# Optimization experiments

Measured on AMD Instinct MI355X. Metric: run time of the kernel, lower is better.

Reference implementation:

```python
import jax, jax.numpy as jnp
import numpy as np

B, S, D, F, E, K = 2, 2048, 1024, 4096, 8, 2

def setup_inputs() -> dict:
    key = jax.random.key(0)
    ks = jax.random.split(key, 5)
    x = jax.random.normal(ks[0], (B, S, D), dtype=jnp.float32)
    Wg = jax.random.normal(ks[1], (D, E), dtype=jnp.float32) * 0.02   # gate (fp32)
    W1 = jax.random.normal(ks[2], (E, D, F), dtype=jnp.float32) * 0.02  # expert fc1
    b1 = jnp.zeros((E, F), dtype=jnp.float32)
    W2 = jax.random.normal(ks[3], (E, F, D), dtype=jnp.float32) * 0.02  # expert fc2
    b2 = jnp.zeros((E, D), dtype=jnp.float32)
    return {"x": x, "Wg": Wg, "W1": W1, "b1": b1, "W2": W2, "b2": b2}

def reference(x, Wg, W1, b1, W2, b2):
    b, s, d = x.shape
    e = Wg.shape[1]
    T = b * s
    C = (2 * K * T) // e  # generous capacity -> effectively no token drops
    xt = x.reshape(T, d)

    # --- top-2 gating (fp32) ---
    logits = xt.astype(jnp.float32) @ Wg.astype(jnp.float32)  # [T,E]
    gates = jax.nn.softmax(logits, axis=-1)
    idx1 = jnp.argmax(gates, axis=-1)                      # [T]
    mask1 = jax.nn.one_hot(idx1, e, dtype=gates.dtype)     # [T,E]
    gate1 = jnp.sum(gates * mask1, axis=-1)                # [T]
    logits2 = jnp.where(mask1 > 0, -jnp.inf, logits)
    idx2 = jnp.argmax(logits2, axis=-1)
    mask2 = jax.nn.one_hot(idx2, e, dtype=gates.dtype)
    gate2 = jnp.sum(gates * mask2, axis=-1)
    denom = gate1 + gate2 + 1e-9
    w1 = gate1 / denom
    w2 = gate2 / denom

    # --- capacity-based slot assignment (GShard-style) ---
    p1 = jnp.cumsum(mask1, axis=0) - mask1                 # earlier same-expert tokens
    pos1 = jnp.sum(p1 * mask1, axis=-1).astype(jnp.int32)  # [T]
    off = jnp.sum(mask1, axis=0)                           # [E] 1st-choice counts
    p2 = jnp.cumsum(mask2, axis=0) - mask2 + off[None, :]
    pos2 = jnp.sum(p2 * mask2, axis=-1).astype(jnp.int32)
    keep1 = (pos1 < C).astype(xt.dtype)
    keep2 = (pos2 < C).astype(xt.dtype)
    pos1 = jnp.clip(pos1, 0, C - 1)
    pos2 = jnp.clip(pos2, 0, C - 1)

    # --- dispatch (scatter tokens to expert slots) ---
    xe = jnp.zeros((e, C, d), dtype=xt.dtype)
    xe = xe.at[idx1, pos1].add(xt * keep1[:, None])
    xe = xe.at[idx2, pos2].add(xt * keep2[:, None])

    # --- grouped expert FFN: gelu(x W1 + b1) W2 + b2 ---
    h = jax.nn.gelu(jnp.einsum('ecd,edf->ecf', xe, W1) + b1[:, None, :], approximate=False)
    ye = jnp.einsum('ecf,efd->ecd', h, W2) + b2[:, None, :]  # [E,C,D]

    # --- combine (gather + weighted sum) ---
    out = ye[idx1, pos1] * (w1 * keep1)[:, None] + ye[idx2, pos2] * (w2 * keep2)[:, None]
    return out.reshape(b, s, d)
```

## Files before the change

kernel.cpp:

```cpp
#include <hip/hip_runtime.h>
#include <hip/hip_bf16.h>
#include <math.h>

#define Dv 1024
#define Fv 4096
#define Ev 8
#define Tt 4096
#define CAP 2048

typedef unsigned int u32;
typedef __bf16 bf16x8 __attribute__((ext_vector_type(8)));
typedef float f32x4 __attribute__((ext_vector_type(4)));

__device__ __forceinline__ unsigned short f2bf(float f) {
  u32 u = __float_as_uint(f);
  u32 r = (u + 0x7fffu + ((u >> 16) & 1u)) >> 16;
  return (unsigned short)r;
}

__device__ __forceinline__ void gload_lds16(const void* g, void* l) {
  __builtin_amdgcn_global_load_lds(
      (const __attribute__((address_space(1))) u32*)g,
      (__attribute__((address_space(3))) u32*)l, 16, 0, 0);
}

__global__ void __launch_bounds__(256)
transpose_bf16_kernel(const float* __restrict__ src, unsigned short* __restrict__ dst,
                      int R, int Cc) {
  __shared__ float tile[64][65];
  int e = blockIdx.z;
  src += (size_t)e * R * Cc;
  dst += (size_t)e * R * Cc;
  int c0 = blockIdx.x * 64, r0 = blockIdx.y * 64;
  int tc = threadIdx.x & 63, tr = threadIdx.x >> 6;
#pragma unroll
  for (int i = tr; i < 64; i += 4)
    tile[i][tc] = src[(size_t)(r0 + i) * Cc + (c0 + tc)];
  __syncthreads();
  int rp = (threadIdx.x & 31) * 2, co = threadIdx.x >> 5;
#pragma unroll
  for (int k = 0; k < 8; ++k) {
    int c = co + 8 * k;
    ushort2 v;
    v.x = f2bf(tile[rp][c]);
    v.y = f2bf(tile[rp + 1][c]);
    *(ushort2*)&dst[(size_t)(c0 + c) * R + (r0 + rp)] = v;
  }
}

__global__ void __launch_bounds__(256)
gating_kernel(const float* __restrict__ x, const float* __restrict__ Wg,
              int* __restrict__ idx1, int* __restrict__ idx2,
              float* __restrict__ w1, float* __restrict__ w2) {
  int t = blockIdx.x * 4 + (threadIdx.x >> 6);
  int lane = threadIdx.x & 63;
  const float* xr = x + (size_t)t * Dv;
  float acc[Ev];
#pragma unroll
  for (int e = 0; e < Ev; ++e) acc[e] = 0.f;
#pragma unroll
  for (int j = 0; j < 4; ++j) {
    int dbase = (lane + 64 * j) * 4;
    float4 xv = *(const float4*)(xr + dbase);
    const float* wr = Wg + (size_t)dbase * Ev;
#pragma unroll
    for (int u = 0; u < 4; ++u) {
      float xd = (&xv.x)[u];
#pragma unroll
      for (int e = 0; e < Ev; ++e) acc[e] += xd * wr[u * Ev + e];
    }
  }
#pragma unroll
  for (int off = 32; off > 0; off >>= 1) {
#pragma unroll
    for (int e = 0; e < Ev; ++e) acc[e] += __shfl_xor(acc[e], off, 64);
  }
  if (lane == 0) {
    float mx = acc[0]; int i1 = 0;
#pragma unroll
    for (int e = 1; e < Ev; ++e) { if (acc[e] > mx) { mx = acc[e]; i1 = e; } }
    float ge[Ev]; float se = 0.f;
#pragma unroll
    for (int e = 0; e < Ev; ++e) { ge[e] = expf(acc[e] - mx); se += ge[e]; }
    float mx2 = -INFINITY; int i2 = 0; bool have = false;
#pragma unroll
    for (int e = 0; e < Ev; ++e) {
      if (e == i1) continue;
      if (!have || acc[e] > mx2) { mx2 = acc[e]; i2 = e; have = true; }
    }
    float g1 = 0.f, g2 = 0.f;
#pragma unroll
    for (int e = 0; e < Ev; ++e) { if (e == i1) g1 = ge[e]; if (e == i2) g2 = ge[e]; }
    g1 /= se; g2 /= se;
    float denom = g1 + g2 + 1e-9f;
    idx1[t] = i1; idx2[t] = i2;
    w1[t] = g1 / denom; w2[t] = g2 / denom;
  }
}

__global__ void __launch_bounds__(256)
scan_kernel(const int* __restrict__ gidx1, const int* __restrict__ gidx2,
            const float* __restrict__ gw1, const float* __restrict__ gw2,
            int* __restrict__ pos1, int* __restrict__ pos2,
            float* __restrict__ w1k, float* __restrict__ w2k,
            int* __restrict__ n_e) {
  __shared__ short s1[Tt], s2[Tt];
  __shared__ int c1[256][Ev], c2[256][Ev];
  __shared__ int tot1[Ev], tot2[Ev];
  int tid = threadIdx.x;
  for (int i = tid; i < Tt; i += 256) { s1[i] = (short)gidx1[i]; s2[i] = (short)gidx2[i]; }
  __syncthreads();
  int base = tid * 16;
  {
    int l1[Ev], l2[Ev];
#pragma unroll
    for (int e = 0; e < Ev; ++e) { l1[e] = 0; l2[e] = 0; }
    for (int j = 0; j < 16; ++j) {
      int a = s1[base + j], b = s2[base + j];
#pragma unroll
      for (int e = 0; e < Ev; ++e) { l1[e] += (a == e); l2[e] += (b == e); }
    }
#pragma unroll
    for (int e = 0; e < Ev; ++e) { c1[tid][e] = l1[e]; c2[tid][e] = l2[e]; }
  }
  __syncthreads();
  if (tid < Ev) {
    int run = 0;
    for (int c = 0; c < 256; ++c) { int v = c1[c][tid]; c1[c][tid] = run; run += v; }
    tot1[tid] = run;
  } else if (tid < 2 * Ev) {
    int e = tid - Ev; int run = 0;
    for (int c = 0; c < 256; ++c) { int v = c2[c][e]; c2[c][e] = run; run += v; }
    tot2[e] = run;
  }
  __syncthreads();
  if (tid < Ev) {
    int ne = tot1[tid] + tot2[tid];
    n_e[tid] = ne < CAP ? ne : CAP;
  }
  int r1[Ev], r2[Ev];
#pragma unroll
  for (int e = 0; e < Ev; ++e) { r1[e] = c1[tid][e]; r2[e] = c2[tid][e] + tot1[e]; }
  for (int j = 0; j < 16; ++j) {
    int tk = base + j;
    int e1 = s1[tk], e2 = s2[tk];
    int p1 = 0, p2 = 0;
#pragma unroll
    for (int e = 0; e < Ev; ++e) {
      if (e == e1) { p1 = r1[e]; r1[e]++; }
      if (e == e2) { p2 = r2[e]; r2[e]++; }
    }
    bool k1 = p1 < CAP, k2 = p2 < CAP;
    pos1[tk] = k1 ? p1 : -1;
    pos2[tk] = k2 ? p2 : -1;
    w1k[tk] = k1 ? gw1[tk] : 0.f;
    w2k[tk] = k2 ? gw2[tk] : 0.f;
  }
}

__global__ void __launch_bounds__(256)
dispatch_kernel(const float* __restrict__ x,
                const int* __restrict__ idx1, const int* __restrict__ idx2,
                const int* __restrict__ pos1, const int* __restrict__ pos2,
                unsigned short* __restrict__ Xe) {
  int t = blockIdx.x, tid = threadIdx.x;
  float4 xv = *(const float4*)(x + (size_t)t * Dv + tid * 4);
  ushort4 bv;
  bv.x = f2bf(xv.x); bv.y = f2bf(xv.y); bv.z = f2bf(xv.z); bv.w = f2bf(xv.w);
  int p1 = pos1[t], p2 = pos2[t];
  int e1 = idx1[t], e2 = idx2[t];
  if (p1 >= 0)
    *(ushort4*)(Xe + ((size_t)(e1 * CAP + p1)) * Dv + tid * 4) = bv;
  if (p2 >= 0)
    *(ushort4*)(Xe + ((size_t)(e2 * CAP + p2)) * Dv + tid * 4) = bv;
}

template <int MODE>
__global__ void __launch_bounds__(256, 2)
gemm_kernel(const unsigned short* __restrict__ A,
            const unsigned short* __restrict__ Bt,
            const float* __restrict__ bias,
            void* __restrict__ Out,
            const int* __restrict__ n_e,
            int M, int N, int K) {
  int e = blockIdx.z;
  int m0 = blockIdx.y * 128, n0 = blockIdx.x * 128;
  if (m0 >= n_e[e]) return;
  A += (size_t)e * M * K;
  Bt += (size_t)e * N * K;
  bias += (size_t)e * N;
  __shared__ unsigned short As[128 * 64];
  __shared__ unsigned short Bs[128 * 64];
  int tid = threadIdx.x;
  int wave = tid >> 6, lane = tid & 63;
  int wm = (wave & 1) * 64, wn = (wave >> 1) * 64;
  int quad = lane >> 4, lr = lane & 15;
  int sw = lr & 7;
  f32x4 acc[4][4];
#pragma unroll
  for (int i = 0; i < 4; ++i)
#pragma unroll
    for (int j = 0; j < 4; ++j)
#pragma unroll
      for (int r = 0; r < 4; ++r) acc[i][j][r] = 0.f;

  int r_st = tid >> 3;
  int g_st = tid & 7;
  int gsrc = g_st ^ (r_st & 7);
  const unsigned short* gA = A + (size_t)(m0 + r_st) * K + gsrc * 8;
  const unsigned short* gB = Bt + (size_t)(n0 + r_st) * K + gsrc * 8;
  unsigned short* lA = &As[tid * 8];
  unsigned short* lB = &Bs[tid * 8];

  for (int k0 = 0; k0 < K; k0 += 64) {
    __syncthreads();
#pragma unroll
    for (int s = 0; s < 4; ++s) {
      gload_lds16(gA + (size_t)(s * 32) * K + k0, lA + s * 2048);
      gload_lds16(gB + (size_t)(s * 32) * K + k0, lB + s * 2048);
    }
    __syncthreads();
#pragma unroll
    for (int h = 0; h < 2; ++h) {
      bf16x8 af[4], bfr[4];
#pragma unroll
      for (int mi = 0; mi < 4; ++mi) {
        int row = wm + mi * 16 + lr;
        int c = (h * 4 + quad) ^ sw;
        af[mi] = *(const bf16x8*)&As[row * 64 + c * 8];
      }
#pragma unroll
      for (int ni = 0; ni < 4; ++ni) {
        int row = wn + ni * 16 + lr;
        int c = (h * 4 + quad) ^ sw;
        bfr[ni] = *(const bf16x8*)&Bs[row * 64 + c * 8];
      }
#pragma unroll
      for (int mi = 0; mi < 4; ++mi)
#pragma unroll
        for (int ni = 0; ni < 4; ++ni)
          acc[mi][ni] = __builtin_amdgcn_mfma_f32_16x16x32_bf16(af[mi], bfr[ni], acc[mi][ni], 0, 0, 0);
    }
  }

#pragma unroll
  for (int ni = 0; ni < 4; ++ni) {
    int col = n0 + wn + ni * 16 + lr;
    float bv = bias[col];
#pragma unroll
    for (int mi = 0; mi < 4; ++mi) {
#pragma unroll
      for (int r = 0; r < 4; ++r) {
        int row = m0 + wm + mi * 16 + quad * 4 + r;
        float v = acc[mi][ni][r] + bv;
        if (MODE == 0) {
          v = 0.5f * v * (1.0f + erff(v * 0.70710678118654752f));
          ((unsigned short*)Out)[((size_t)e * M + row) * N + col] = f2bf(v);
        } else {
          ((float*)Out)[((size_t)e * M + row) * N + col] = v;
        }
      }
    }
  }
}

__global__ void __launch_bounds__(256)
combine_kernel(const float* __restrict__ ye,
               const int* __restrict__ idx1, const int* __restrict__ idx2,
               const int* __restrict__ pos1, const int* __restrict__ pos2,
               const float* __restrict__ w1k, const float* __restrict__ w2k,
               float* __restrict__ out) {
  int t = blockIdx.x, tid = threadIdx.x;
  int p1 = pos1[t], p2 = pos2[t];
  float a1 = w1k[t], a2 = w2k[t];
  float4 o = make_float4(0.f, 0.f, 0.f, 0.f);
  if (p1 >= 0) {
    float4 y = *(const float4*)(ye + ((size_t)(idx1[t] * CAP + p1)) * Dv + tid * 4);
    o.x += a1 * y.x; o.y += a1 * y.y; o.z += a1 * y.z; o.w += a1 * y.w;
  }
  if (p2 >= 0) {
    float4 y = *(const float4*)(ye + ((size_t)(idx2[t] * CAP + p2)) * Dv + tid * 4);
    o.x += a2 * y.x; o.y += a2 * y.y; o.z += a2 * y.z; o.w += a2 * y.w;
  }
  *(float4*)(out + (size_t)t * Dv + tid * 4) = o;
}

extern "C" void kernel_launch(void* const* d_in, const int* in_sizes, int n_in,
                              void* d_out, int out_size, void* d_ws, size_t ws_size,
                              hipStream_t stream) {
  const float* x  = (const float*)d_in[0];
  const float* Wg = (const float*)d_in[1];
  const float* W1 = (const float*)d_in[2];
  const float* b1 = (const float*)d_in[3];
  const float* W2 = (const float*)d_in[4];
  const float* b2 = (const float*)d_in[5];
  float* out = (float*)d_out;

  char* p = (char*)d_ws;
  size_t off = 0;
  auto alloc = [&](size_t bytes) {
    void* q = p + off;
    off += (bytes + 255) & ~(size_t)255;
    return q;
  };
  unsigned short* Wt1 = (unsigned short*)alloc((size_t)Ev * Fv * Dv * 2);
  unsigned short* Wt2 = (unsigned short*)alloc((size_t)Ev * Dv * Fv * 2);
  unsigned short* Xe  = (unsigned short*)alloc((size_t)Ev * CAP * Dv * 2);
  unsigned short* h   = (unsigned short*)alloc((size_t)Ev * CAP * Fv * 2);
  int*   idx1 = (int*)alloc(Tt * 4);
  int*   idx2 = (int*)alloc(Tt * 4);
  int*   pos1 = (int*)alloc(Tt * 4);
  int*   pos2 = (int*)alloc(Tt * 4);
  float* w1   = (float*)alloc(Tt * 4);
  float* w2   = (float*)alloc(Tt * 4);
  float* w1k  = (float*)alloc(Tt * 4);
  float* w2k  = (float*)alloc(Tt * 4);
  int*   n_e  = (int*)alloc(Ev * 4);
  float* ye   = (float*)Wt1;

  transpose_bf16_kernel<<<dim3(Fv / 64, Dv / 64, Ev), 256, 0, stream>>>(W1, Wt1, Dv, Fv);
  transpose_bf16_kernel<<<dim3(Dv / 64, Fv / 64, Ev), 256, 0, stream>>>(W2, Wt2, Fv, Dv);
  gating_kernel<<<Tt / 4, 256, 0, stream>>>(x, Wg, idx1, idx2, w1, w2);
  scan_kernel<<<1, 256, 0, stream>>>(idx1, idx2, w1, w2, pos1, pos2, w1k, w2k, n_e);
  dispatch_kernel<<<Tt, 256, 0, stream>>>(x, idx1, idx2, pos1, pos2, Xe);
  gemm_kernel<0><<<dim3(Fv / 128, CAP / 128, Ev), 256, 0, stream>>>(
      Xe, Wt1, b1, h, n_e, CAP, Fv, Dv);
  gemm_kernel<1><<<dim3(Dv / 128, CAP / 128, Ev), 256, 0, stream>>>(
      h, Wt2, b2, ye, n_e, CAP, Dv, Fv);
  combine_kernel<<<Tt, 256, 0, stream>>>(ye, idx1, idx2, pos1, pos2, w1k, w2k, out);
}
```

Before: 622.0 us.

## Pack expert rows contiguously, split-K the second GEMM, reorder grid and launches

Routed tokens are now stored in one packed buffer of rows, with per-expert base offsets computed in the scan, so the GEMMs index compact rows and skip padded capacity rows in their epilogue. The second GEMM splits K into two halves that write separate fp32 partial buffers, and the combine kernel sums them. This gives more blocks to fill the GPU. The grid puts experts on blockIdx.x so that row tiles of different experts interleave, and the W2 transpose moves after the first GEMM. The cost is extra fp32 partial writes and reads in exchange for better occupancy and less wasted tile work.

```diff
diff --git a/kernel.cpp b/kernel.cpp
--- a/kernel.cpp
+++ b/kernel.cpp
@@ -7,6 +7,8 @@
 #define Ev 8
 #define Tt 4096
 #define CAP 2048
+#define NROW 8192
+#define RPAD 128
 
 typedef unsigned int u32;
 typedef __bf16 bf16x8 __attribute__((ext_vector_type(8)));
@@ -101,12 +103,12 @@
 __global__ void __launch_bounds__(256)
 scan_kernel(const int* __restrict__ gidx1, const int* __restrict__ gidx2,
             const float* __restrict__ gw1, const float* __restrict__ gw2,
-            int* __restrict__ pos1, int* __restrict__ pos2,
+            int* __restrict__ ci1, int* __restrict__ ci2,
             float* __restrict__ w1k, float* __restrict__ w2k,
-            int* __restrict__ n_e) {
+            int* __restrict__ n_e, int* __restrict__ base_e) {
   __shared__ short s1[Tt], s2[Tt];
   __shared__ int c1[256][Ev], c2[256][Ev];
-  __shared__ int tot1[Ev], tot2[Ev];
+  __shared__ int tot1[Ev], tot2[Ev], sne[Ev], sbase[Ev];
   int tid = threadIdx.x;
   for (int i = tid; i < Tt; i += 256) { s1[i] = (short)gidx1[i]; s2[i] = (short)gidx2[i]; }
   __syncthreads();
@@ -124,20 +126,26 @@
     for (int e = 0; e < Ev; ++e) { c1[tid][e] = l1[e]; c2[tid][e] = l2[e]; }
   }
   __syncthreads();
-  if (tid < Ev) {
+  if (tid < 2 * Ev) {
+    int e = tid & 7;
+    int* col = (tid < Ev) ? &c1[0][e] : &c2[0][e];
     int run = 0;
-    for (int c = 0; c < 256; ++c) { int v = c1[c][tid]; c1[c][tid] = run; run += v; }
-    tot1[tid] = run;
-  } else if (tid < 2 * Ev) {
-    int e = tid - Ev; int run = 0;
-    for (int c = 0; c < 256; ++c) { int v = c2[c][e]; c2[c][e] = run; run += v; }
-    tot2[e] = run;
-  }
-  __syncthreads();
-  if (tid < Ev) {
-    int ne = tot1[tid] + tot2[tid];
-    n_e[tid] = ne < CAP ? ne : CAP;
-  }
+    for (int c = 0; c < 256; ++c) { int v = col[(size_t)c * Ev]; col[(size_t)c * Ev] = run; run += v; }
+    if (tid < Ev) tot1[e] = run; else tot2[e] = run;
+  }
+  __syncthreads();
+  if (tid == 0) {
+    int b = 0;
+#pragma unroll
+    for (int e = 0; e < Ev; ++e) {
+      int ne = tot1[e] + tot2[e];
+      ne = ne < CAP ? ne : CAP;
+      sne[e] = ne; sbase[e] = b;
+      n_e[e] = ne; base_e[e] = b;
+      b += ne;
+    }
+  }
+  __syncthreads();
   int r1[Ev], r2[Ev];
 #pragma unroll
   for (int e = 0; e < Ev; ++e) { r1[e] = c1[tid][e]; r2[e] = c2[tid][e] + tot1[e]; }
@@ -151,8 +159,8 @@
       if (e == e2) { p2 = r2[e]; r2[e]++; }
     }
     bool k1 = p1 < CAP, k2 = p2 < CAP;
-    pos1[tk] = k1 ? p1 : -1;
-    pos2[tk] = k2 ? p2 : -1;
+    ci1[tk] = k1 ? (sbase[e1] + p1) : -1;
+    ci2[tk] = k2 ? (sbase[e2] + p2) : -1;
     w1k[tk] = k1 ? gw1[tk] : 0.f;
     w2k[tk] = k2 ? gw2[tk] : 0.f;
   }
@@ -160,35 +168,38 @@
 
 __global__ void __launch_bounds__(256)
 dispatch_kernel(const float* __restrict__ x,
-                const int* __restrict__ idx1, const int* __restrict__ idx2,
-                const int* __restrict__ pos1, const int* __restrict__ pos2,
+                const int* __restrict__ ci1, const int* __restrict__ ci2,
                 unsigned short* __restrict__ Xe) {
   int t = blockIdx.x, tid = threadIdx.x;
   float4 xv = *(const float4*)(x + (size_t)t * Dv + tid * 4);
   ushort4 bv;
   bv.x = f2bf(xv.x); bv.y = f2bf(xv.y); bv.z = f2bf(xv.z); bv.w = f2bf(xv.w);
-  int p1 = pos1[t], p2 = pos2[t];
-  int e1 = idx1[t], e2 = idx2[t];
-  if (p1 >= 0)
-    *(ushort4*)(Xe + ((size_t)(e1 * CAP + p1)) * Dv + tid * 4) = bv;
-  if (p2 >= 0)
-    *(ushort4*)(Xe + ((size_t)(e2 * CAP + p2)) * Dv + tid * 4) = bv;
-}
-
-template <int MODE>
+  int c1 = ci1[t], c2 = ci2[t];
+  if (c1 >= 0) *(ushort4*)(Xe + (size_t)c1 * Dv + tid * 4) = bv;
+  if (c2 >= 0) *(ushort4*)(Xe + (size_t)c2 * Dv + tid * 4) = bv;
+}
+
+template <int MODE, int SPLITS>
 __global__ void __launch_bounds__(256, 2)
 gemm_kernel(const unsigned short* __restrict__ A,
             const unsigned short* __restrict__ Bt,
             const float* __restrict__ bias,
             void* __restrict__ Out,
-            const int* __restrict__ n_e,
-            int M, int N, int K) {
-  int e = blockIdx.z;
-  int m0 = blockIdx.y * 128, n0 = blockIdx.x * 128;
-  if (m0 >= n_e[e]) return;
-  A += (size_t)e * M * K;
-  Bt += (size_t)e * N * K;
+            const int* __restrict__ n_e, const int* __restrict__ base_e,
+            int N, int K) {
+  int e = blockIdx.x;
+  int zz = blockIdx.z;
+  int split = zz % SPLITS, mt = zz / SPLITS;
+  int m0 = mt * 128;
+  int ne = n_e[e];
+  if (m0 >= ne) return;
+  int rbase = base_e[e];
+  int n0 = blockIdx.y * 128;
+  const int kchunk = K / SPLITS;
+  A += ((size_t)(rbase + m0)) * K + (size_t)split * kchunk;
+  Bt += (size_t)e * N * K + (size_t)n0 * K + (size_t)split * kchunk;
   bias += (size_t)e * N;
+
   __shared__ unsigned short As[128 * 64];
   __shared__ unsigned short Bs[128 * 64];
   int tid = threadIdx.x;
@@ -207,12 +218,12 @@
   int r_st = tid >> 3;
   int g_st = tid & 7;
   int gsrc = g_st ^ (r_st & 7);
-  const unsigned short* gA = A + (size_t)(m0 + r_st) * K + gsrc * 8;
-  const unsigned short* gB = Bt + (size_t)(n0 + r_st) * K + gsrc * 8;
+  const unsigned short* gA = A + (size_t)r_st * K + gsrc * 8;
+  const unsigned short* gB = Bt + (size_t)r_st * K + gsrc * 8;
   unsigned short* lA = &As[tid * 8];
   unsigned short* lB = &Bs[tid * 8];
 
-  for (int k0 = 0; k0 < K; k0 += 64) {
+  for (int k0 = 0; k0 < kchunk; k0 += 64) {
     __syncthreads();
 #pragma unroll
     for (int s = 0; s < 4; ++s) {
@@ -246,18 +257,21 @@
 #pragma unroll
   for (int ni = 0; ni < 4; ++ni) {
     int col = n0 + wn + ni * 16 + lr;
-    float bv = bias[col];
+    float bv = (MODE == 0 || split == 0) ? bias[col] : 0.f;
 #pragma unroll
     for (int mi = 0; mi < 4; ++mi) {
 #pragma unroll
       for (int r = 0; r < 4; ++r) {
-        int row = m0 + wm + mi * 16 + quad * 4 + r;
-        float v = acc[mi][ni][r] + bv;
-        if (MODE == 0) {
-          v = 0.5f * v * (1.0f + erff(v * 0.70710678118654752f));
-          ((unsigned short*)Out)[((size_t)e * M + row) * N + col] = f2bf(v);
-        } else {
-          ((float*)Out)[((size_t)e * M + row) * N + col] = v;
+        int rowl = m0 + wm + mi * 16 + quad * 4 + r;
+        if (rowl < ne) {
+          size_t grow = (size_t)(rbase + rowl);
+          float v = acc[mi][ni][r] + bv;
+          if (MODE == 0) {
+            v = 0.5f * v * (1.0f + erff(v * 0.70710678118654752f));
+            ((unsigned short*)Out)[grow * N + col] = f2bf(v);
+          } else {
+            ((float*)Out)[((size_t)split * NROW + grow) * N + col] = v;
+          }
         }
       }
     }
@@ -266,21 +280,25 @@
 
 __global__ void __launch_bounds__(256)
 combine_kernel(const float* __restrict__ ye,
-               const int* __restrict__ idx1, const int* __restrict__ idx2,
-               const int* __restrict__ pos1, const int* __restrict__ pos2,
+               const int* __restrict__ ci1, const int* __restrict__ ci2,
                const float* __restrict__ w1k, const float* __restrict__ w2k,
                float* __restrict__ out) {
   int t = blockIdx.x, tid = threadIdx.x;
-  int p1 = pos1[t], p2 = pos2[t];
+  int c1 = ci1[t], c2 = ci2[t];
   float a1 = w1k[t], a2 = w2k[t];
+  const float* ye1 = ye + (size_t)NROW * Dv;
   float4 o = make_float4(0.f, 0.f, 0.f, 0.f);
-  if (p1 >= 0) {
-    float4 y = *(const float4*)(ye + ((size_t)(idx1[t] * CAP + p1)) * Dv + tid * 4);
-    o.x += a1 * y.x; o.y += a1 * y.y; o.z += a1 * y.z; o.w += a1 * y.w;
-  }
-  if (p2 >= 0) {
-    float4 y = *(const float4*)(ye + ((size_t)(idx2[t] * CAP + p2)) * Dv + tid * 4);
-    o.x += a2 * y.x; o.y += a2 * y.y; o.z += a2 * y.z; o.w += a2 * y.w;
+  if (c1 >= 0) {
+    float4 y0 = *(const float4*)(ye + (size_t)c1 * Dv + tid * 4);
+    float4 y1 = *(const float4*)(ye1 + (size_t)c1 * Dv + tid * 4);
+    o.x += a1 * (y0.x + y1.x); o.y += a1 * (y0.y + y1.y);
+    o.z += a1 * (y0.z + y1.z); o.w += a1 * (y0.w + y1.w);
+  }
+  if (c2 >= 0) {
+    float4 y0 = *(const float4*)(ye + (size_t)c2 * Dv + tid * 4);
+    float4 y1 = *(const float4*)(ye1 + (size_t)c2 * Dv + tid * 4);
+    o.x += a2 * (y0.x + y1.x); o.y += a2 * (y0.y + y1.y);
+    o.z += a2 * (y0.z + y1.z); o.w += a2 * (y0.w + y1.w);
   }
   *(float4*)(out + (size_t)t * Dv + tid * 4) = o;
 }
@@ -305,27 +323,28 @@
   };
   unsigned short* Wt1 = (unsigned short*)alloc((size_t)Ev * Fv * Dv * 2);
   unsigned short* Wt2 = (unsigned short*)alloc((size_t)Ev * Dv * Fv * 2);
-  unsigned short* Xe  = (unsigned short*)alloc((size_t)Ev * CAP * Dv * 2);
-  unsigned short* h   = (unsigned short*)alloc((size_t)Ev * CAP * Fv * 2);
+  unsigned short* Xe  = (unsigned short*)alloc((size_t)(NROW + RPAD) * Dv * 2);
+  unsigned short* h   = (unsigned short*)alloc((size_t)(NROW + RPAD) * Fv * 2);
   int*   idx1 = (int*)alloc(Tt * 4);
   int*   idx2 = (int*)alloc(Tt * 4);
-  int*   pos1 = (int*)alloc(Tt * 4);
-  int*   pos2 = (int*)alloc(Tt * 4);
+  int*   ci1  = (int*)alloc(Tt * 4);
+  int*   ci2  = (int*)alloc(Tt * 4);
   float* w1   = (float*)alloc(Tt * 4);
   float* w2   = (float*)alloc(Tt * 4);
   float* w1k  = (float*)alloc(Tt * 4);
   float* w2k  = (float*)alloc(Tt * 4);
   int*   n_e  = (int*)alloc(Ev * 4);
+  int*   base = (int*)alloc(Ev * 4);
   float* ye   = (float*)Wt1;
 
   transpose_bf16_kernel<<<dim3(Fv / 64, Dv / 64, Ev), 256, 0, stream>>>(W1, Wt1, Dv, Fv);
+  gating_kernel<<<Tt / 4, 256, 0, stream>>>(x, Wg, idx1, idx2, w1, w2);
+  scan_kernel<<<1, 256, 0, stream>>>(idx1, idx2, w1, w2, ci1, ci2, w1k, w2k, n_e, base);
+  dispatch_kernel<<<Tt, 256, 0, stream>>>(x, ci1, ci2, Xe);
+  gemm_kernel<0, 1><<<dim3(Ev, Fv / 128, CAP / 128), 256, 0, stream>>>(
+      Xe, Wt1, b1, h, n_e, base, Fv, Dv);
   transpose_bf16_kernel<<<dim3(Dv / 64, Fv / 64, Ev), 256, 0, stream>>>(W2, Wt2, Fv, Dv);
-  gating_kernel<<<Tt / 4, 256, 0, stream>>>(x, Wg, idx1, idx2, w1, w2);
-  scan_kernel<<<1, 256, 0, stream>>>(idx1, idx2, w1, w2, pos1, pos2, w1k, w2k, n_e);
-  dispatch_kernel<<<Tt, 256, 0, stream>>>(x, idx1, idx2, pos1, pos2, Xe);
-  gemm_kernel<0><<<dim3(Fv / 128, CAP / 128, Ev), 256, 0, stream>>>(
-      Xe, Wt1, b1, h, n_e, CAP, Fv, Dv);
-  gemm_kernel<1><<<dim3(Dv / 128, CAP / 128, Ev), 256, 0, stream>>>(
-      h, Wt2, b2, ye, n_e, CAP, Dv, Fv);
-  combine_kernel<<<Tt, 256, 0, stream>>>(ye, idx1, idx2, pos1, pos2, w1k, w2k, out);
-}
+  gemm_kernel<1, 2><<<dim3(Ev, Dv / 128, (CAP / 128) * 2), 256, 0, stream>>>(
+      h, Wt2, b2, ye, n_e, base, Dv, Fv);
+  combine_kernel<<<Tt, 256, 0, stream>>>(ye, ci1, ci2, w1k, w2k, out);
+}
```

Result: no change. 634.4 us (+2.0%).
